# Kernel optimization log

Measured on AMD Instinct MI355X. Metric: run time of the kernel, lower is better.

Reference implementation:

```python
import jax, jax.numpy as jnp
import numpy as np

B, N, D = 4, 2048, 512
H = 8
DH = D // H
FF = 2 * D


def setup_inputs() -> dict:
    key = jax.random.key(0)
    ks = jax.random.split(key, 16)
    s = lambda fan_in: 1.0 / np.sqrt(fan_in)
    inp = {
        "x0": jax.random.normal(ks[0], (B, N, D), jnp.float32),
        "x1": jax.random.normal(ks[1], (B, N, D), jnp.float32),
        # projections (torch Linear: weight [out, in])
        "Wqk": jax.random.uniform(ks[2], (D, D), jnp.float32, -s(D), s(D)),
        "bqk": jax.random.uniform(ks[3], (D,), jnp.float32, -s(D), s(D)),
        "Wv": jax.random.uniform(ks[4], (D, D), jnp.float32, -s(D), s(D)),
        "bv": jax.random.uniform(ks[5], (D,), jnp.float32, -s(D), s(D)),
        "Wo": jax.random.uniform(ks[6], (D, D), jnp.float32, -s(D), s(D)),
        "bo": jax.random.uniform(ks[7], (D,), jnp.float32, -s(D), s(D)),
        # FFN: Linear(2D,2D) -> LayerNorm(2D) -> GELU -> Linear(2D,D)
        "Wf1": jax.random.uniform(ks[8], (FF, FF), jnp.float32, -s(FF), s(FF)),
        "bf1": jax.random.uniform(ks[9], (FF,), jnp.float32, -s(FF), s(FF)),
        "ln_g": jnp.ones((FF,), jnp.float32),
        "ln_b": jnp.zeros((FF,), jnp.float32),
        "Wf2": jax.random.uniform(ks[10], (D, FF), jnp.float32, -s(FF), s(FF)),
        "bf2": jax.random.uniform(ks[11], (D,), jnp.float32, -s(FF), s(FF)),
    }
    return inp


def _split_heads(t):
    # [B,N,D] -> [B,H,N,DH]
    return t.reshape(B, N, H, DH).transpose(0, 2, 1, 3)


def _attn(q, k, v):
    # q,k,v: [B,H,N,DH]; scale by sqrt(d_k) as in the torch Attention module
    scores = jnp.einsum("bhnd,bhmd->bhnm", q, k) / jnp.sqrt(jnp.float32(DH))
    attn = jax.nn.softmax(scores, axis=-1)
    return jnp.einsum("bhnm,bhmd->bhnd", attn, v)


def _merge_heads(t):
    # [B,H,N,DH] -> [B,N,D]
    return t.transpose(0, 2, 1, 3).reshape(B, N, D)


def _ffn(x, Wf1, bf1, ln_g, ln_b, Wf2, bf2):
    h = x @ Wf1.T + bf1
    mu = jnp.mean(h, axis=-1, keepdims=True)
    var = jnp.mean(jnp.square(h - mu), axis=-1, keepdims=True)
    h = (h - mu) / jnp.sqrt(var + 1e-5) * ln_g + ln_b
    h = jax.nn.gelu(h, approximate=False)
    return h @ Wf2.T + bf2


def reference(x0, x1, Wqk, bqk, Wv, bv, Wo, bo, Wf1, bf1, ln_g, ln_b, Wf2, bf2):
    qk0 = _split_heads(x0 @ Wqk.T + bqk)
    qk1 = _split_heads(x1 @ Wqk.T + bqk)
    v0 = _split_heads(x0 @ Wv.T + bv)
    v1 = _split_heads(x1 @ Wv.T + bv)

    m0 = _merge_heads(_attn(qk0, qk1, v1)) @ Wo.T + bo
    m1 = _merge_heads(_attn(qk1, qk0, v0)) @ Wo.T + bo

    y0 = x0 + _ffn(jnp.concatenate([x0, m0], -1), Wf1, bf1, ln_g, ln_b, Wf2, bf2)
    y1 = x1 + _ffn(jnp.concatenate([x1, m1], -1), Wf1, bf1, ln_g, ln_b, Wf2, bf2)
    return (y0, y1)
```

## Files before the change

### kernel.cpp

```cpp
#include <hip/hip_runtime.h>
#include <hip/hip_bf16.h>
#include <math.h>

typedef __bf16 bf16;
typedef __bf16 bf16x8 __attribute__((ext_vector_type(8)));
typedef __bf16 bf16x4 __attribute__((ext_vector_type(4)));
typedef float  f32x4  __attribute__((ext_vector_type(4)));
typedef float  f32x16 __attribute__((ext_vector_type(16)));
typedef unsigned int u32x2 __attribute__((ext_vector_type(2)));

#define DEVI __device__ __forceinline__

DEVI void async16(bf16* lds, const bf16* g) {
    __builtin_amdgcn_global_load_lds(
        (const __attribute__((address_space(1))) unsigned int*)g,
        (__attribute__((address_space(3))) unsigned int*)lds, 16, 0, 0);
}
DEVI f32x4 mfma16(bf16x8 a, bf16x8 b, f32x4 c) {
    return __builtin_amdgcn_mfma_f32_16x16x32_bf16(a, b, c, 0, 0, 0);
}
DEVI f32x16 mfma32(bf16x8 a, bf16x8 b, f32x16 c) {
    return __builtin_amdgcn_mfma_f32_32x32x16_bf16(a, b, c, 0, 0, 0);
}
DEVI unsigned cvtpk(float lo, float hi) {
    unsigned r;
    asm("v_cvt_pk_bf16_f32 %0, %1, %2" : "=v"(r) : "v"(lo), "v"(hi));
    return r;
}
DEVI void pl32(unsigned &a, unsigned &b) {
    u32x2 r = __builtin_amdgcn_permlane32_swap(a, b, false, false);
    a = r.x; b = r.y;
}
DEVI bf16x8 mk8(unsigned a0, unsigned a1, unsigned b0, unsigned b1) {
    union { unsigned u[4]; bf16x8 v; } U;
    U.u[0] = a0; U.u[1] = a1; U.u[2] = b0; U.u[3] = b1;
    return U.v;
}

__global__ __launch_bounds__(256) void prep(
    const float* __restrict__ x0, const float* __restrict__ x1, bf16* __restrict__ Xbf,
    const float* __restrict__ Wqk, const float* __restrict__ Wv,
    const float* __restrict__ Wf1, const float* __restrict__ Wf2,
    bf16* __restrict__ Wqkv, bf16* __restrict__ Wbig, bf16* __restrict__ Wf1Rb,
    bf16* __restrict__ Wf2b,
    const float* __restrict__ Wo, bf16* __restrict__ WoT,
    const float* __restrict__ bo, const float* __restrict__ bf1,
    float* __restrict__ bf1p)
{
    __shared__ float Ls[64][65];
    const int bid = blockIdx.x, t = threadIdx.x;
    if (bid < 8192) {
        long i = (long)bid * 256 + t;
        long r = i >> 7, c = (i & 127) * 4;
        const float* src = (r < 8192) ? (x0 + r * 512 + c) : (x1 + (r - 8192) * 512 + c);
        float4 v = *(const float4*)src;
        bf16x4 o;
        o[0] = (bf16)v.x; o[1] = (bf16)v.y; o[2] = (bf16)v.z; o[3] = (bf16)v.w;
        *(bf16x4*)(Xbf + r * 1024 + c) = o;
    } else if (bid < 10240) {
        long i = (long)(bid - 8192) * 256 + t;
        const float* s; bf16* d;
        if (i < 131072) {
            s = (i < 65536) ? Wqk + i * 4 : Wv + (i - 65536) * 4;
            d = Wqkv + i * 4;
        } else if (i < 393216) {
            long e = (i - 131072) * 4, r = e >> 10, c = e & 1023;
            s = Wf1 + e;
            d = (c < 512) ? (Wbig + r * 1024 + c) : (Wf1Rb + r * 512 + (c - 512));
        } else {
            s = Wf2 + (i - 393216) * 4;
            d = Wf2b + (i - 393216) * 4;
        }
        float4 v = *(const float4*)s;
        bf16x4 o;
        o[0] = (bf16)v.x; o[1] = (bf16)v.y; o[2] = (bf16)v.z; o[3] = (bf16)v.w;
        *(bf16x4*)d = o;
    } else if (bid < 10304) {
        const int bb = bid - 10240;
        const int bi = bb & 7, bj = bb >> 3;
        const int i0 = bi * 64, j0 = bj * 64;
        const int r0 = t >> 4, c4 = (t & 15) * 4;
#pragma unroll
        for (int it = 0; it < 4; it++) {
            int row = r0 + 16 * it;
            float4 v = *(const float4*)(Wo + (long)(i0 + row) * 512 + j0 + c4);
            Ls[row][c4] = v.x; Ls[row][c4 + 1] = v.y;
            Ls[row][c4 + 2] = v.z; Ls[row][c4 + 3] = v.w;
        }
        __syncthreads();
#pragma unroll
        for (int it = 0; it < 4; it++) {
            int orow = r0 + 16 * it;
            bf16x4 o;
#pragma unroll
            for (int k = 0; k < 4; k++) o[k] = (bf16)Ls[c4 + k][orow];
            *(bf16x4*)(WoT + (long)(j0 + orow) * 512 + i0 + c4) = o;
        }
    } else {
        const int w = t >> 6, lane = t & 63;
        const int row = (bid - 10304) * 4 + w;
        const float* rp = Wf1 + (long)row * 1024 + 512 + lane * 8;
        float4 a = *(const float4*)rp;
        float4 b = *(const float4*)(rp + 4);
        const float* bp = bo + lane * 8;
        float4 c = *(const float4*)bp;
        float4 d = *(const float4*)(bp + 4);
        float s = a.x * c.x + a.y * c.y + a.z * c.z + a.w * c.w +
                  b.x * d.x + b.y * d.y + b.z * d.z + b.w * d.w;
#pragma unroll
        for (int k = 1; k < 64; k <<= 1) s += __shfl_xor(s, k);
        if (lane == 0) bf1p[row] = bf1[row] + s;
    }
}

template <int MODE>
__global__ __launch_bounds__(256) void gemm_bt(
    const bf16* __restrict__ A, long lda,
    const bf16* __restrict__ B, long ldb,
    const float* __restrict__ bias,
    void* __restrict__ Cout, long ldc,
    const float* __restrict__ res0, const float* __restrict__ res1,
    const float* __restrict__ bias2, void* __restrict__ Cout2,
    int M, int N, int K, float scale)
{
    __shared__ bf16 As[128 * 64];
    __shared__ bf16 Bs[128 * 64];
    const int t = threadIdx.x;
    const int w = t >> 6, lane = t & 63, quad = lane >> 4, m15 = lane & 15;
    const int wm = w >> 1, wn = w & 1;
    const int nbx = N >> 7;
    const int xcd = blockIdx.x & 7, local = blockIdx.x >> 3;
    const int mtiles_per_xcd = (int)(gridDim.x >> 3) / nbx;
    const int by = xcd * mtiles_per_xcd + local / nbx;
    const int bx = local % nbx;
    const long m0 = (long)by * 128, n0 = (long)bx * 128;

    f32x4 acc[4][4] = {};

    for (int k0 = 0; k0 < K; k0 += 64) {
#pragma unroll
        for (int i = 0; i < 4; i++) {
            int idx = i * 256 + t, row = idx >> 3, p = idx & 7;
            int gc = k0 + ((p ^ (row & 7)) * 8);
            async16(As + idx * 8, A + (m0 + row) * lda + gc);
            async16(Bs + idx * 8, B + (n0 + row) * ldb + gc);
        }
        __syncthreads();
#pragma unroll
        for (int kk = 0; kk < 2; kk++) {
            bf16x8 af[4], bfr[4];
#pragma unroll
            for (int mt = 0; mt < 4; mt++) {
                int row = wm * 64 + mt * 16 + m15;
                af[mt] = *(const bf16x8*)(As + row * 64 + (((kk * 4 + quad) ^ (row & 7)) * 8));
            }
#pragma unroll
            for (int nt = 0; nt < 4; nt++) {
                int row = wn * 64 + nt * 16 + m15;
                bfr[nt] = *(const bf16x8*)(Bs + row * 64 + (((kk * 4 + quad) ^ (row & 7)) * 8));
            }
#pragma unroll
            for (int mt = 0; mt < 4; mt++)
#pragma unroll
                for (int nt = 0; nt < 4; nt++)
                    acc[mt][nt] = mfma16(af[mt], bfr[nt], acc[mt][nt]);
        }
        __syncthreads();
    }

#pragma unroll
    for (int nt = 0; nt < 4; nt++) {
        long col = n0 + wn * 64 + nt * 16 + m15;
#pragma unroll
        for (int mt = 0; mt < 4; mt++) {
            long row = m0 + wm * 64 + mt * 16 + quad * 4;
            if (MODE == 0) {
                bf16* C = (bf16*)Cout;
                float bs = bias[col];
#pragma unroll
                for (int r = 0; r < 4; r++)
                    C[(row + r) * ldc + col] = (bf16)(acc[mt][nt][r] + bs);
            } else if (MODE == 4) {
                bf16* C = (bf16*)Cout;
#pragma unroll
                for (int r = 0; r < 4; r++)
                    C[(row + r) * ldc + col] = (bf16)acc[mt][nt][r];
            } else if (MODE == 5) {
                if (col < 512) {
                    bf16* C = (bf16*)Cout;
                    float bs = bias[col];
#pragma unroll
                    for (int r = 0; r < 4; r++)
                        C[(row + r) * ldc + col] = (bf16)((acc[mt][nt][r] + bs) * scale);
                } else {
                    bf16* V = (bf16*)Cout2;
                    long v = col - 512;
                    float bs = bias2[v];
                    bf16x4 pv;
#pragma unroll
                    for (int r = 0; r < 4; r++) pv[r] = (bf16)(acc[mt][nt][r] + bs);
                    *(bf16x4*)(V + v * 16384 + row) = pv;
                }
            } else {
                float* C = (float*)Cout;
                float bs = bias[col];
#pragma unroll
                for (int r = 0; r < 4; r++) {
                    long grow = row + r;
                    const float* rs = (grow < 8192) ? (res0 + grow * 512)
                                                    : (res1 + (grow - 8192) * 512);
                    C[grow * ldc + col] = acc[mt][nt][r] + bs + rs[col];
                }
            }
        }
    }
}

__global__ __launch_bounds__(256, 4) void flash_attn(const bf16* __restrict__ QK,
                                                     const bf16* __restrict__ VT,
                                                     bf16* __restrict__ o)
{
    __shared__ bf16 lds[16384];

    const int t = threadIdx.x, w = t >> 6, lane = t & 63;
    const int l31 = lane & 31, hi = lane >> 5;
    const int j = blockIdx.x;
    const int hs = j & 63;
    const int qt = j >> 6;
    const int h = hs & 7, b = (hs >> 3) & 3, dir = hs >> 5;
    const long qrow0  = (long)dir * 8192 + b * 2048 + qt * 128;
    const long kvrow0 = (long)(1 - dir) * 8192 + b * 2048;
    const int hc = h * 64;

#pragma unroll
    for (int i = 0; i < 4; i++) {
        int idx = i * 256 + t, row = idx >> 3, p = idx & 7;
        async16(lds + idx * 8, QK + (qrow0 + row) * 512 + hc + ((p ^ (row & 7)) * 8));
    }
    __syncthreads();
    bf16x8 qf[4];
    {
        int qrow = w * 32 + l31;
#pragma unroll
        for (int kd = 0; kd < 4; kd++)
            qf[kd] = *(const bf16x8*)(lds + qrow * 64 + (((kd * 2 + hi) ^ (qrow & 7)) * 8));
    }
    __syncthreads();

#pragma unroll
    for (int i = 0; i < 2; i++) {
        int idx = i * 256 + t, row = idx >> 3, p = idx & 7;
        async16(lds + idx * 8, QK + (kvrow0 + row) * 512 + hc + ((p ^ (row & 7)) * 8));
    }
#pragma unroll
    for (int i = 0; i < 2; i++) {
        int idx = i * 256 + t, row = idx >> 3, p = idx & 7;
        async16(lds + 8192 + idx * 8, VT + (long)(hc + row) * 16384 + kvrow0 + ((p ^ (row & 7)) * 8));
    }

    f32x16 oacc[2] = {};
    f32x16 racc = {};
    bf16x8 ones;
#pragma unroll
    for (int k = 0; k < 8; k++) ones[k] = (bf16)1.0f;

    for (int kb = 0; kb < 32; kb++) {
        bf16* Kc = lds + (kb & 1) * 4096;
        bf16* Vc = lds + 8192 + (kb & 1) * 4096;

        asm volatile("s_waitcnt vmcnt(0)" ::: "memory");
        __builtin_amdgcn_s_barrier();

        if (kb < 31) {
            const long knext = kvrow0 + (kb + 1) * 64;
            bf16* Kn = lds + ((kb + 1) & 1) * 4096;
            bf16* Vn = lds + 8192 + ((kb + 1) & 1) * 4096;
#pragma unroll
            for (int i = 0; i < 2; i++) {
                int idx = i * 256 + t, row = idx >> 3, p = idx & 7;
                async16(Kn + idx * 8, QK + (knext + row) * 512 + hc + ((p ^ (row & 7)) * 8));
            }
#pragma unroll
            for (int i = 0; i < 2; i++) {
                int idx = i * 256 + t, row = idx >> 3, p = idx & 7;
                async16(Vn + idx * 8, VT + (long)(hc + row) * 16384 + knext + ((p ^ (row & 7)) * 8));
            }
        }

#pragma unroll
        for (int kb2 = 0; kb2 < 2; kb2++) {
            const int krow = kb2 * 32 + l31;
            const int ksw = krow & 7;
            bf16x8 kf0 = *(const bf16x8*)(Kc + krow * 64 + (((0 + hi) ^ ksw) * 8));
            bf16x8 kf1 = *(const bf16x8*)(Kc + krow * 64 + (((2 + hi) ^ ksw) * 8));
            bf16x8 kf2 = *(const bf16x8*)(Kc + krow * 64 + (((4 + hi) ^ ksw) * 8));
            bf16x8 kf3 = *(const bf16x8*)(Kc + krow * 64 + (((6 + hi) ^ ksw) * 8));

            f32x16 s0 = {};
            __builtin_amdgcn_s_setprio(1);
            s0 = mfma32(kf0, qf[0], s0);
            s0 = mfma32(kf1, qf[1], s0);
            s0 = mfma32(kf2, qf[2], s0);
            s0 = mfma32(kf3, qf[3], s0);
            __builtin_amdgcn_s_setprio(0);

#pragma unroll
            for (int r = 0; r < 16; r++) s0[r] = exp2f(s0[r]);

#pragma unroll
            for (int sh = 0; sh < 2; sh++) {
                const int ks = kb2 * 2 + sh;
                unsigned a00 = cvtpk(s0[8 * sh + 0], s0[8 * sh + 1]);
                unsigned a01 = cvtpk(s0[8 * sh + 2], s0[8 * sh + 3]);
                unsigned b00 = cvtpk(s0[8 * sh + 4], s0[8 * sh + 5]);
                unsigned b01 = cvtpk(s0[8 * sh + 6], s0[8 * sh + 7]);
                pl32(a00, b00); pl32(a01, b01);
                bf16x8 pa0 = mk8(a00, a01, b00, b01);

                __builtin_amdgcn_s_setprio(1);
#pragma unroll
                for (int db = 0; db < 2; db++) {
                    const int vrow = db * 32 + l31;
                    bf16x8 vf = *(const bf16x8*)(Vc + vrow * 64 + (((ks * 2 + hi) ^ (vrow & 7)) * 8));
                    oacc[db] = mfma32(pa0, vf, oacc[db]);
                }
                racc = mfma32(pa0, ones, racc);
                __builtin_amdgcn_s_setprio(0);
            }
        }
    }

#pragma unroll
    for (int reg = 0; reg < 16; reg++) {
        const int q = (reg & 3) + 8 * (reg >> 2) + 4 * hi;
        const float inv = 1.f / racc[reg];
        const long row = qrow0 + w * 32 + q;
#pragma unroll
        for (int db = 0; db < 2; db++)
            o[row * 1024 + hc + db * 32 + l31] = (bf16)(oacc[db][reg] * inv);
    }
}

__global__ __launch_bounds__(256) void ln_gelu(bf16* __restrict__ H,
                                               const float* __restrict__ g,
                                               const float* __restrict__ bta)
{
    const int row = blockIdx.x, t = threadIdx.x;
    const int w = t >> 6, lane = t & 63;
    bf16* hp = H + (long)row * 1024 + t * 4;
    bf16x4 hv = *(const bf16x4*)hp;
    float h[4];
#pragma unroll
    for (int j = 0; j < 4; j++) h[j] = (float)hv[j];
    float s1 = h[0] + h[1] + h[2] + h[3];
    float s2 = h[0] * h[0] + h[1] * h[1] + h[2] * h[2] + h[3] * h[3];
#pragma unroll
    for (int d = 1; d < 64; d <<= 1) {
        s1 += __shfl_xor(s1, d);
        s2 += __shfl_xor(s2, d);
    }
    __shared__ float rbuf[8];
    if (lane == 0) { rbuf[w] = s1; rbuf[4 + w] = s2; }
    __syncthreads();
    s1 = rbuf[0] + rbuf[1] + rbuf[2] + rbuf[3];
    s2 = rbuf[4] + rbuf[5] + rbuf[6] + rbuf[7];
    const float mu = s1 * (1.f / 1024.f);
    const float var = s2 * (1.f / 1024.f) - mu * mu;
    const float rstd = rsqrtf(var + 1e-5f);
    bf16x4 out;
#pragma unroll
    for (int j = 0; j < 4; j++) {
        int c = t * 4 + j;
        float x = (h[j] - mu) * rstd * g[c] + bta[c];
        float y = 0.5f * x * (1.f + erff(x * 0.70710678118654752f));
        out[j] = (bf16)y;
    }
    *(bf16x4*)hp = out;
}

extern "C" void kernel_launch(void* const* d_in, const int* in_sizes, int n_in,
                              void* d_out, int out_size, void* d_ws, size_t ws_size,
                              hipStream_t stream)
{
    const float* x0  = (const float*)d_in[0];
    const float* x1  = (const float*)d_in[1];
    const float* Wqk = (const float*)d_in[2];
    const float* bqk = (const float*)d_in[3];
    const float* Wv  = (const float*)d_in[4];
    const float* bv  = (const float*)d_in[5];
    const float* Wo  = (const float*)d_in[6];
    const float* bo  = (const float*)d_in[7];
    const float* Wf1 = (const float*)d_in[8];
    const float* bf1 = (const float*)d_in[9];
    const float* lng = (const float*)d_in[10];
    const float* lnb = (const float*)d_in[11];
    const float* Wf2 = (const float*)d_in[12];
    const float* bf2 = (const float*)d_in[13];

    char* ws = (char*)d_ws;
    bf16* Xbf   = (bf16*)ws; ws += 16384L * 1024 * 2;
    bf16* QKbf  = (bf16*)ws;
    bf16* Hbuf  = (bf16*)ws;
    ws += 16384L * 512 * 2;
    bf16* VtG   = (bf16*)ws; ws += 16384L * 512 * 2;
    bf16* Wqkv  = (bf16*)ws; ws += 1024L * 512 * 2;
    bf16* Wbig  = (bf16*)ws; ws += 1024L * 1024 * 2;
    bf16* Wf1Rb = (bf16*)ws; ws += 1024L * 512 * 2;
    bf16* Wf2b  = (bf16*)ws; ws += 512L * 1024 * 2;
    bf16* WoT   = (bf16*)ws; ws += 512L * 512 * 2;
    float* bf1p = (float*)ws; ws += 1024 * 4;

    const float qs = 0.42466090014400953f;

    prep<<<10560, 256, 0, stream>>>(x0, x1, Xbf, Wqk, Wv, Wf1, Wf2,
                                    Wqkv, Wbig, Wf1Rb, Wf2b, Wo, WoT, bo, bf1, bf1p);

    gemm_bt<4><<<32, 256, 0, stream>>>(Wf1Rb, 512, WoT, 512, nullptr,
                                       Wbig + 512, 1024, nullptr, nullptr,
                                       nullptr, nullptr, 1024, 512, 512, 1.f);

    gemm_bt<5><<<1024, 256, 0, stream>>>(Xbf, 1024, Wqkv, 512, bqk,
                                         QKbf, 512, nullptr, nullptr,
                                         bv, VtG, 16384, 1024, 512, qs);

    flash_attn<<<1024, 256, 0, stream>>>(QKbf, VtG, Xbf + 512);

    gemm_bt<0><<<1024, 256, 0, stream>>>(Xbf, 1024, Wbig, 1024, bf1p,
                                         Hbuf, 1024, nullptr, nullptr,
                                         nullptr, nullptr, 16384, 1024, 1024, 1.f);
    ln_gelu<<<16384, 256, 0, stream>>>(Hbuf, lng, lnb);
    gemm_bt<1><<<512, 256, 0, stream>>>(Hbuf, 1024, Wf2b, 1024, bf2,
                                        d_out, 512, x0, x1,
                                        nullptr, nullptr, 16384, 512, 1024, 1.f);
}
```

Before: 362.5 us.

## Rewrite flash attention as single-wave blocks loading K/V directly from global

The attention kernel moves from 256-thread blocks with double-buffered LDS staging of K and V to 64-thread blocks. Each wave now handles 64 query rows and loads its K and V fragments straight from global memory into registers, with no shared memory or barriers. The row-sum is no longer computed by an extra MFMA against a ones vector. It is accumulated in scalar adds and reduced with shuffles. The trade is that K/V reuse across waves through LDS is lost, so global and L2 traffic rises and load latency is exposed, in exchange for removing barrier syncs and one MFMA per step.

```diff
diff --git a/kernel.cpp b/kernel.cpp
--- a/kernel.cpp
+++ b/kernel.cpp
@@ -216,128 +216,102 @@
     }
 }
 
-__global__ __launch_bounds__(256, 4) void flash_attn(const bf16* __restrict__ QK,
-                                                     const bf16* __restrict__ VT,
-                                                     bf16* __restrict__ o)
+__global__ __launch_bounds__(64, 2) void flash_attn(const bf16* __restrict__ QK,
+                                                    const bf16* __restrict__ VT,
+                                                    bf16* __restrict__ o)
 {
-    __shared__ bf16 lds[16384];
-
-    const int t = threadIdx.x, w = t >> 6, lane = t & 63;
+    const int lane = threadIdx.x;
     const int l31 = lane & 31, hi = lane >> 5;
     const int j = blockIdx.x;
     const int hs = j & 63;
     const int qt = j >> 6;
     const int h = hs & 7, b = (hs >> 3) & 3, dir = hs >> 5;
-    const long qrow0  = (long)dir * 8192 + b * 2048 + qt * 128;
+    const long qrow0  = (long)dir * 8192 + b * 2048 + qt * 64;
     const long kvrow0 = (long)(1 - dir) * 8192 + b * 2048;
     const int hc = h * 64;
 
-#pragma unroll
-    for (int i = 0; i < 4; i++) {
-        int idx = i * 256 + t, row = idx >> 3, p = idx & 7;
-        async16(lds + idx * 8, QK + (qrow0 + row) * 512 + hc + ((p ^ (row & 7)) * 8));
-    }
-    __syncthreads();
-    bf16x8 qf[4];
-    {
-        int qrow = w * 32 + l31;
+    const bf16* qp = QK + (qrow0 + l31) * 512 + hc + hi * 8;
+    bf16x8 qf[2][4];
+#pragma unroll
+    for (int qb = 0; qb < 2; qb++)
 #pragma unroll
         for (int kd = 0; kd < 4; kd++)
-            qf[kd] = *(const bf16x8*)(lds + qrow * 64 + (((kd * 2 + hi) ^ (qrow & 7)) * 8));
-    }
-    __syncthreads();
-
-#pragma unroll
-    for (int i = 0; i < 2; i++) {
-        int idx = i * 256 + t, row = idx >> 3, p = idx & 7;
-        async16(lds + idx * 8, QK + (kvrow0 + row) * 512 + hc + ((p ^ (row & 7)) * 8));
-    }
-#pragma unroll
-    for (int i = 0; i < 2; i++) {
-        int idx = i * 256 + t, row = idx >> 3, p = idx & 7;
-        async16(lds + 8192 + idx * 8, VT + (long)(hc + row) * 16384 + kvrow0 + ((p ^ (row & 7)) * 8));
-    }
-
-    f32x16 oacc[2] = {};
-    f32x16 racc = {};
-    bf16x8 ones;
-#pragma unroll
-    for (int k = 0; k < 8; k++) ones[k] = (bf16)1.0f;
+            qf[qb][kd] = *(const bf16x8*)(qp + qb * (32 * 512) + kd * 16);
+
+    const bf16* kp = QK + (kvrow0 + l31) * 512 + hc + hi * 8;
+    const bf16* vp = VT + (long)(hc + l31) * 16384 + kvrow0 + hi * 8;
+
+    f32x16 oacc[2][2] = {};
+    float rs0 = 0.f, rs1 = 0.f;
 
     for (int kb = 0; kb < 32; kb++) {
-        bf16* Kc = lds + (kb & 1) * 4096;
-        bf16* Vc = lds + 8192 + (kb & 1) * 4096;
-
-        asm volatile("s_waitcnt vmcnt(0)" ::: "memory");
-        __builtin_amdgcn_s_barrier();
-
-        if (kb < 31) {
-            const long knext = kvrow0 + (kb + 1) * 64;
-            bf16* Kn = lds + ((kb + 1) & 1) * 4096;
-            bf16* Vn = lds + 8192 + ((kb + 1) & 1) * 4096;
-#pragma unroll
-            for (int i = 0; i < 2; i++) {
-                int idx = i * 256 + t, row = idx >> 3, p = idx & 7;
-                async16(Kn + idx * 8, QK + (knext + row) * 512 + hc + ((p ^ (row & 7)) * 8));
+        const long ko = (long)kb * 64;
+        bf16x8 vf[4][2];
+#pragma unroll
+        for (int ks = 0; ks < 4; ks++)
+#pragma unroll
+            for (int db = 0; db < 2; db++)
+                vf[ks][db] = *(const bf16x8*)(vp + db * (32L * 16384) + ko + ks * 16);
+
+#pragma unroll
+        for (int kb2 = 0; kb2 < 2; kb2++) {
+            const bf16* kbp = kp + (ko + kb2 * 32) * 512;
+            bf16x8 kf0 = *(const bf16x8*)(kbp);
+            bf16x8 kf1 = *(const bf16x8*)(kbp + 16);
+            bf16x8 kf2 = *(const bf16x8*)(kbp + 32);
+            bf16x8 kf3 = *(const bf16x8*)(kbp + 48);
+
+#pragma unroll
+            for (int qb = 0; qb < 2; qb++) {
+                f32x16 s0 = {};
+                __builtin_amdgcn_s_setprio(1);
+                s0 = mfma32(kf0, qf[qb][0], s0);
+                s0 = mfma32(kf1, qf[qb][1], s0);
+                s0 = mfma32(kf2, qf[qb][2], s0);
+                s0 = mfma32(kf3, qf[qb][3], s0);
+                __builtin_amdgcn_s_setprio(0);
+
+#pragma unroll
+                for (int r = 0; r < 16; r++) s0[r] = exp2f(s0[r]);
+                float ls = (((s0[0] + s0[1]) + (s0[2] + s0[3])) +
+                            ((s0[4] + s0[5]) + (s0[6] + s0[7]))) +
+                           (((s0[8] + s0[9]) + (s0[10] + s0[11])) +
+                            ((s0[12] + s0[13]) + (s0[14] + s0[15])));
+                if (qb == 0) rs0 += ls; else rs1 += ls;
+
+#pragma unroll
+                for (int sh = 0; sh < 2; sh++) {
+                    unsigned a0 = cvtpk(s0[8 * sh + 0], s0[8 * sh + 1]);
+                    unsigned a1 = cvtpk(s0[8 * sh + 2], s0[8 * sh + 3]);
+                    unsigned b0 = cvtpk(s0[8 * sh + 4], s0[8 * sh + 5]);
+                    unsigned b1 = cvtpk(s0[8 * sh + 6], s0[8 * sh + 7]);
+                    pl32(a0, b0); pl32(a1, b1);
+                    bf16x8 pa = mk8(a0, a1, b0, b1);
+                    const int ks = kb2 * 2 + sh;
+                    __builtin_amdgcn_s_setprio(1);
+                    oacc[qb][0] = mfma32(pa, vf[ks][0], oacc[qb][0]);
+                    oacc[qb][1] = mfma32(pa, vf[ks][1], oacc[qb][1]);
+                    __builtin_amdgcn_s_setprio(0);
+                }
             }
-#pragma unroll
-            for (int i = 0; i < 2; i++) {
-                int idx = i * 256 + t, row = idx >> 3, p = idx & 7;
-                async16(Vn + idx * 8, VT + (long)(hc + row) * 16384 + knext + ((p ^ (row & 7)) * 8));
-            }
-        }
-
-#pragma unroll
-        for (int kb2 = 0; kb2 < 2; kb2++) {
-            const int krow = kb2 * 32 + l31;
-            const int ksw = krow & 7;
-            bf16x8 kf0 = *(const bf16x8*)(Kc + krow * 64 + (((0 + hi) ^ ksw) * 8));
-            bf16x8 kf1 = *(const bf16x8*)(Kc + krow * 64 + (((2 + hi) ^ ksw) * 8));
-            bf16x8 kf2 = *(const bf16x8*)(Kc + krow * 64 + (((4 + hi) ^ ksw) * 8));
-            bf16x8 kf3 = *(const bf16x8*)(Kc + krow * 64 + (((6 + hi) ^ ksw) * 8));
-
-            f32x16 s0 = {};
-            __builtin_amdgcn_s_setprio(1);
-            s0 = mfma32(kf0, qf[0], s0);
-            s0 = mfma32(kf1, qf[1], s0);
-            s0 = mfma32(kf2, qf[2], s0);
-            s0 = mfma32(kf3, qf[3], s0);
-            __builtin_amdgcn_s_setprio(0);
-
-#pragma unroll
-            for (int r = 0; r < 16; r++) s0[r] = exp2f(s0[r]);
-
-#pragma unroll
-            for (int sh = 0; sh < 2; sh++) {
-                const int ks = kb2 * 2 + sh;
-                unsigned a00 = cvtpk(s0[8 * sh + 0], s0[8 * sh + 1]);
-                unsigned a01 = cvtpk(s0[8 * sh + 2], s0[8 * sh + 3]);
-                unsigned b00 = cvtpk(s0[8 * sh + 4], s0[8 * sh + 5]);
-                unsigned b01 = cvtpk(s0[8 * sh + 6], s0[8 * sh + 7]);
-                pl32(a00, b00); pl32(a01, b01);
-                bf16x8 pa0 = mk8(a00, a01, b00, b01);
-
-                __builtin_amdgcn_s_setprio(1);
-#pragma unroll
-                for (int db = 0; db < 2; db++) {
-                    const int vrow = db * 32 + l31;
-                    bf16x8 vf = *(const bf16x8*)(Vc + vrow * 64 + (((ks * 2 + hi) ^ (vrow & 7)) * 8));
-                    oacc[db] = mfma32(pa0, vf, oacc[db]);
-                }
-                racc = mfma32(pa0, ones, racc);
-                __builtin_amdgcn_s_setprio(0);
-            }
-        }
-    }
-
+        }
+    }
+
+    rs0 += __shfl_xor(rs0, 32);
+    rs1 += __shfl_xor(rs1, 32);
+    const float inv0 = 1.f / rs0;
+    const float inv1 = 1.f / rs1;
 #pragma unroll
     for (int reg = 0; reg < 16; reg++) {
         const int q = (reg & 3) + 8 * (reg >> 2) + 4 * hi;
-        const float inv = 1.f / racc[reg];
-        const long row = qrow0 + w * 32 + q;
-#pragma unroll
-        for (int db = 0; db < 2; db++)
-            o[row * 1024 + hc + db * 32 + l31] = (bf16)(oacc[db][reg] * inv);
+        const float iq0 = __shfl(inv0, q);
+        const float iq1 = __shfl(inv1, q);
+        const long row0 = qrow0 + q;
+        const long row1 = qrow0 + 32 + q;
+        o[row0 * 1024 + hc + l31]      = (bf16)(oacc[0][0][reg] * iq0);
+        o[row0 * 1024 + hc + 32 + l31] = (bf16)(oacc[0][1][reg] * iq0);
+        o[row1 * 1024 + hc + l31]      = (bf16)(oacc[1][0][reg] * iq1);
+        o[row1 * 1024 + hc + 32 + l31] = (bf16)(oacc[1][1][reg] * iq1);
     }
 }
 
@@ -423,7 +397,7 @@
                                          QKbf, 512, nullptr, nullptr,
                                          bv, VtG, 16384, 1024, 512, qs);
 
-    flash_attn<<<1024, 256, 0, stream>>>(QKbf, VtG, Xbf + 512);
+    flash_attn<<<2048, 64, 0, stream>>>(QKbf, VtG, Xbf + 512);
 
     gemm_bt<0><<<1024, 256, 0, stream>>>(Xbf, 1024, Wbig, 1024, bf1p,
                                          Hbuf, 1024, nullptr, nullptr,
```

New measurement: 390.4 us. 1.08x slower.

## Add double-buffered 256x256 pipelined GEMM for QKV and FFN1 projections

Applied to the files above, without the earlier changes.

Adds a new pipe_gemm kernel with 256x256 output tiles, 512 threads, XOR-swizzled LDS, and a two-stage async global-to-LDS prefetch pipeline with raised MFMA priority. It also remaps blocks per XCD so each chiplet works on contiguous M tiles. It replaces gemm_bt for the fused QK/V projection and the first FFN GEMM, aiming at more operand reuse per tile and at hiding load latency. The cost is 128KB of LDS and fewer, larger blocks: 256 blocks on roughly 256 CUs leaves little room for latency hiding across blocks.

```diff
diff --git a/kernel.cpp b/kernel.cpp
--- a/kernel.cpp
+++ b/kernel.cpp
@@ -185,31 +185,135 @@
 #pragma unroll
                 for (int r = 0; r < 4; r++)
                     C[(row + r) * ldc + col] = (bf16)acc[mt][nt][r];
-            } else if (MODE == 5) {
+            } else {
+                float* C = (float*)Cout;
+                float bs = bias[col];
+#pragma unroll
+                for (int r = 0; r < 4; r++) {
+                    long grow = row + r;
+                    const float* rs = (grow < 8192) ? (res0 + grow * 512)
+                                                    : (res1 + (grow - 8192) * 512);
+                    C[grow * ldc + col] = acc[mt][nt][r] + bs + rs[col];
+                }
+            }
+        }
+    }
+}
+
+template <int MODE>
+__global__ __launch_bounds__(512, 2) void pipe_gemm(
+    const bf16* __restrict__ A, long lda,
+    const bf16* __restrict__ B, long ldb,
+    const float* __restrict__ bias,
+    void* __restrict__ Cout, long ldc,
+    const float* __restrict__ bias2, void* __restrict__ Cout2,
+    int M, int N, int K, float scale)
+{
+    __shared__ bf16 lds[65536];
+    bf16* As = lds;
+    bf16* Bs = lds + 32768;
+
+    const int t = threadIdx.x;
+    const int w = t >> 6, lane = t & 63, quad = lane >> 4, m15 = lane & 15;
+    const int wm = w >> 2, wn = w & 3;
+    const int nbx = N >> 8;
+    const int xcd = blockIdx.x & 7, local = blockIdx.x >> 3;
+    const int mtiles_per_xcd = (int)(gridDim.x >> 3) / nbx;
+    const int by = xcd * mtiles_per_xcd + local / nbx;
+    const int bx = local % nbx;
+    const long m0 = (long)by * 256, n0 = (long)bx * 256;
+    const int nt = K >> 6;
+
+    f32x4 acc[8][4] = {};
+
+    auto stage = [&](int kt) {
+        const int slot = kt & 1;
+        bf16* Ad = As + slot * 16384;
+        bf16* Bd = Bs + slot * 16384;
+        const int k0 = kt * 64;
+#pragma unroll
+        for (int i = 0; i < 4; i++) {
+            int idx = i * 512 + t, row = idx >> 3, p = idx & 7;
+            int gc = k0 + ((p ^ (row & 7)) * 8);
+            async16(Ad + idx * 8, A + (m0 + row) * lda + gc);
+        }
+#pragma unroll
+        for (int i = 0; i < 4; i++) {
+            int idx = i * 512 + t, row = idx >> 3, p = idx & 7;
+            int gc = k0 + ((p ^ (row & 7)) * 8);
+            async16(Bd + idx * 8, B + (n0 + row) * ldb + gc);
+        }
+    };
+
+    stage(0);
+    stage(1);
+
+    for (int kt = 0; kt < nt; kt++) {
+        if (kt + 1 < nt) {
+            asm volatile("s_waitcnt vmcnt(8)" ::: "memory");
+        } else {
+            asm volatile("s_waitcnt vmcnt(0)" ::: "memory");
+        }
+        __builtin_amdgcn_s_barrier();
+        __builtin_amdgcn_sched_barrier(0);
+
+        const bf16* Asl = As + (kt & 1) * 16384;
+        const bf16* Bsl = Bs + (kt & 1) * 16384;
+#pragma unroll
+        for (int ksub = 0; ksub < 2; ksub++) {
+            bf16x8 af[8], bfr[4];
+#pragma unroll
+            for (int mf = 0; mf < 8; mf++) {
+                int row = wm * 128 + mf * 16 + m15;
+                af[mf] = *(const bf16x8*)(Asl + row * 64 + (((ksub * 4 + quad) ^ (row & 7)) * 8));
+            }
+#pragma unroll
+            for (int nf = 0; nf < 4; nf++) {
+                int row = wn * 64 + nf * 16 + m15;
+                bfr[nf] = *(const bf16x8*)(Bsl + row * 64 + (((ksub * 4 + quad) ^ (row & 7)) * 8));
+            }
+            __builtin_amdgcn_s_setprio(1);
+#pragma unroll
+            for (int mf = 0; mf < 8; mf++)
+#pragma unroll
+                for (int nf = 0; nf < 4; nf++)
+                    acc[mf][nf] = mfma16(af[mf], bfr[nf], acc[mf][nf]);
+            __builtin_amdgcn_s_setprio(0);
+        }
+
+        __builtin_amdgcn_sched_barrier(0);
+        __builtin_amdgcn_s_barrier();
+        __builtin_amdgcn_sched_barrier(0);
+        if (kt + 2 < nt) stage(kt + 2);
+    }
+
+#pragma unroll
+    for (int nf = 0; nf < 4; nf++) {
+        long col = n0 + wn * 64 + nf * 16 + m15;
+#pragma unroll
+        for (int mf = 0; mf < 8; mf++) {
+            long row = m0 + wm * 128 + mf * 16 + quad * 4;
+            if (MODE == 0) {
+                bf16* C = (bf16*)Cout;
+                float bs = bias[col];
+#pragma unroll
+                for (int r = 0; r < 4; r++)
+                    C[(row + r) * ldc + col] = (bf16)(acc[mf][nf][r] + bs);
+            } else {
                 if (col < 512) {
                     bf16* C = (bf16*)Cout;
                     float bs = bias[col];
 #pragma unroll
                     for (int r = 0; r < 4; r++)
-                        C[(row + r) * ldc + col] = (bf16)((acc[mt][nt][r] + bs) * scale);
+                        C[(row + r) * ldc + col] = (bf16)((acc[mf][nf][r] + bs) * scale);
                 } else {
                     bf16* V = (bf16*)Cout2;
                     long v = col - 512;
                     float bs = bias2[v];
                     bf16x4 pv;
 #pragma unroll
-                    for (int r = 0; r < 4; r++) pv[r] = (bf16)(acc[mt][nt][r] + bs);
+                    for (int r = 0; r < 4; r++) pv[r] = (bf16)(acc[mf][nf][r] + bs);
                     *(bf16x4*)(V + v * 16384 + row) = pv;
-                }
-            } else {
-                float* C = (float*)Cout;
-                float bs = bias[col];
-#pragma unroll
-                for (int r = 0; r < 4; r++) {
-                    long grow = row + r;
-                    const float* rs = (grow < 8192) ? (res0 + grow * 512)
-                                                    : (res1 + (grow - 8192) * 512);
-                    C[grow * ldc + col] = acc[mt][nt][r] + bs + rs[col];
                 }
             }
         }
@@ -419,15 +523,15 @@
                                        Wbig + 512, 1024, nullptr, nullptr,
                                        nullptr, nullptr, 1024, 512, 512, 1.f);
 
-    gemm_bt<5><<<1024, 256, 0, stream>>>(Xbf, 1024, Wqkv, 512, bqk,
-                                         QKbf, 512, nullptr, nullptr,
-                                         bv, VtG, 16384, 1024, 512, qs);
+    pipe_gemm<5><<<256, 512, 0, stream>>>(Xbf, 1024, Wqkv, 512, bqk,
+                                          QKbf, 512, bv, VtG,
+                                          16384, 1024, 512, qs);
 
     flash_attn<<<1024, 256, 0, stream>>>(QKbf, VtG, Xbf + 512);
 
-    gemm_bt<0><<<1024, 256, 0, stream>>>(Xbf, 1024, Wbig, 1024, bf1p,
-                                         Hbuf, 1024, nullptr, nullptr,
-                                         nullptr, nullptr, 16384, 1024, 1024, 1.f);
+    pipe_gemm<0><<<256, 512, 0, stream>>>(Xbf, 1024, Wbig, 1024, bf1p,
+                                          Hbuf, 1024, nullptr, nullptr,
+                                          16384, 1024, 1024, 1.f);
     ln_gelu<<<16384, 256, 0, stream>>>(Hbuf, lng, lnb);
     gemm_bt<1><<<512, 256, 0, stream>>>(Hbuf, 1024, Wf2b, 1024, bf2,
                                         d_out, 512, x0, x1,
```

After: 353.3 us. -2.5%, faster.
